# Kernel optimization log

Hardware: AMD Instinct MI355X
Metric: run time of the kernel (lower is better)

The kernel has to match this reference:

```python
import jax, jax.numpy as jnp
import numpy as np

B, S = 4, 4096
D_MODEL = 1024
INDEXER_DIM = 64
LOCAL_WINDOW = 16
MEDIUM_WINDOW = 64
GLOBAL_K = 32
LOCAL_SPARSE = 0.8


def _local_k_schedule(seq_len):
    # Replicates torch: k_local = max(1, int(L * (1 - local_sparse))) with Python float math
    ks = []
    for q in range(seq_len):
        L = min(q + 1, LOCAL_WINDOW)
        ks.append(max(1, int(L * (1.0 - LOCAL_SPARSE))))
    ks = np.asarray(ks, dtype=np.int32)
    return ks, int(ks.max())


def setup_inputs() -> dict:
    key = jax.random.key(0)
    kx, kl, km, kg = jax.random.split(key, 4)
    scale = D_MODEL ** -0.5
    return {
        "x": jax.random.normal(kx, (B, S, D_MODEL), jnp.float32),
        "W_local": jax.random.normal(kl, (INDEXER_DIM, D_MODEL), jnp.float32) * scale,
        "W_medium": jax.random.normal(km, (INDEXER_DIM, D_MODEL), jnp.float32) * scale,
        "W_global": jax.random.normal(kg, (INDEXER_DIM, D_MODEL), jnp.float32) * scale,
    }


def reference(x, W_local, W_medium, W_global):
    Bb, Ss, _ = x.shape
    neg_inf = jnp.array(-jnp.inf, x.dtype)
    zero = jnp.array(0.0, x.dtype)

    lf = x @ W_local.T   # [B,S,i]
    mf = x @ W_medium.T  # computed by the original but DEAD: medium branch never fires
    gf = x @ W_global.T  # [B,S,i]

    mask = jnp.full((Bb, 1, Ss, Ss), -jnp.inf, x.dtype)
    q_ix = jnp.arange(Ss)
    b_ix = jnp.arange(Bb)[:, None, None]
    qq = q_ix[None, :, None]

    # ---- local scale: causal window [max(0, q-W+1), q] ----
    offs = jnp.arange(LOCAL_WINDOW)
    win = q_ix[:, None] - (LOCAL_WINDOW - 1) + offs[None, :]  # [S,W] absolute key positions
    valid = win >= 0
    winc = jnp.clip(win, 0, Ss - 1)
    lwin = lf[:, winc]                                        # [B,S,W,i]
    lscores = jax.nn.relu(jnp.einsum('bqd,bqwd->bqw', lf, lwin))
    lscores = jnp.where(valid[None], lscores, -jnp.inf)
    ks, kmax = _local_k_schedule(Ss)
    _, tl = jax.lax.top_k(lscores, kmax)                      # [B,S,kmax] window-relative
    labs = jnp.take_along_axis(jnp.broadcast_to(winc[None], (Bb, Ss, LOCAL_WINDOW)), tl, axis=-1)
    keep = jnp.arange(kmax)[None, None, :] < jnp.asarray(ks)[None, :, None]  # [1,S,kmax]
    lvals = jnp.where(keep, zero, neg_inf)
    mask = mask.at[b_ix, 0, qq, labs].max(jnp.broadcast_to(lvals, labs.shape))

    # ---- medium scale: DEAD CODE in the original (medium_end == local_end always) ----

    # ---- global scale (active because seq_len > medium_window and global_k > 0) ----
    if Ss > MEDIUM_WINDOW and GLOBAL_K > 0:
        gs = jax.nn.relu(jnp.einsum('bqd,bkd->bqk', gf, gf))  # [B,S,S]
        j = jnp.arange(Ss)[None, :]
        banned = (j <= q_ix[:, None]) & (j >= q_ix[:, None] - (LOCAL_WINDOW - 1))  # [S,S]
        gs = jnp.where(banned[None], -jnp.inf, gs)
        _, tg = jax.lax.top_k(gs, GLOBAL_K)                   # [B,S,Kg]
        mask = mask.at[b_ix, 0, qq, tg].max(jnp.zeros(tg.shape, x.dtype))

    return mask
```

## Files before the change

kernel.cpp:

```cpp
#include <hip/hip_runtime.h>
#include <hip/hip_fp16.h>
#include <cstdint>

#define SEQ 4096
#define NB 4
#define DMODEL 1024
#define ID 64
#define LW 16
#define GK 32
#define TQ 4

#define NEG_INF (-__builtin_inff())
#define MASKED4 0xFBFFFBFFu
#define FMAT (NB * SEQ * ID)

typedef _Float16 f16x8 __attribute__((ext_vector_type(8)));
typedef float f32x4 __attribute__((ext_vector_type(4)));

__global__ __launch_bounds__(256)
void hp_feat_v10(const unsigned short* __restrict__ xu,
                 const unsigned short* __restrict__ Wlu,
                 const unsigned short* __restrict__ Wgu,
                 float* __restrict__ lf, float* __restrict__ gfT)
{
    const int tid = threadIdx.x;
    const int lane = tid & 63, w = tid >> 6;
    const int half = blockIdx.x & 1;
    const long row0 = (long)(blockIdx.x >> 1) * 64;
    const _Float16* xp = (const _Float16*)xu;
    const _Float16* Wp = (const _Float16*)(half ? Wgu : Wlu);

    const int lr = lane & 15;
    const int kg = lane >> 4;

    const _Float16* ap = xp + (row0 + w * 16 + lr) * DMODEL + kg * 8;
    const _Float16* bp = Wp + (long)lr * DMODEL + kg * 8;

    f32x4 acc[4];
#pragma unroll
    for (int ct = 0; ct < 4; ct++) acc[ct] = (f32x4){0.f, 0.f, 0.f, 0.f};

#pragma unroll 4
    for (int k0 = 0; k0 < DMODEL; k0 += 32) {
        f16x8 av = *(const f16x8*)(ap + k0);
#pragma unroll
        for (int ct = 0; ct < 4; ct++) {
            f16x8 bv = *(const f16x8*)(bp + (long)ct * 16 * DMODEL + k0);
            acc[ct] = __builtin_amdgcn_mfma_f32_16x16x32_f16(av, bv, acc[ct], 0, 0, 0);
        }
    }

    if (!half) {
#pragma unroll
        for (int ct = 0; ct < 4; ct++)
#pragma unroll
            for (int r = 0; r < 4; r++)
                lf[(row0 + w * 16 + kg * 4 + r) * ID + ct * 16 + lr] = acc[ct][r];
    } else {
        const int bb = (int)(row0 >> 12), s0 = (int)(row0 & 4095);
#pragma unroll
        for (int ct = 0; ct < 4; ct++) {
            float4 st = make_float4(acc[ct][0], acc[ct][1], acc[ct][2], acc[ct][3]);
            *(float4*)(gfT + ((long)bb * ID + ct * 16 + lr) * SEQ
                           + s0 + w * 16 + kg * 4) = st;
        }
    }
}

__global__ __launch_bounds__(512)
void hp_mask_v10(const float* __restrict__ lf, const float* __restrict__ gfT,
                 unsigned short* __restrict__ out)
{
    __shared__ float qv[TQ][ID];
    __shared__ float lq[TQ][ID];
    __shared__ unsigned long long red[4][8];
    __shared__ unsigned int bitmap[TQ][SEQ / 32];
    __shared__ float lsc[TQ][LW];
    __shared__ unsigned short tm[512];

    const int tid = threadIdx.x;
    const int lane = tid & 63, w = tid >> 6;
    const int bq = blockIdx.x;
    const int b = bq >> 10;
    const int q0 = (bq & 1023) * TQ;
    const float* gTb = gfT + (long)b * ID * SEQ;
    const float* lfb = lf + (long)b * SEQ * ID;

    if (tid < 256) {
        int d = tid >> 2, qi = tid & 3;
        qv[qi][d] = gTb[(long)d * SEQ + q0 + qi];
        int qi2 = tid >> 6, d2 = tid & 63;
        lq[qi2][d2] = lfb[(long)(q0 + qi2) * ID + d2];
    }
    ((unsigned int*)bitmap)[tid] = 0u;
    __syncthreads();

    float acc[2][4][TQ];
#pragma unroll
    for (int c = 0; c < 2; c++)
#pragma unroll
        for (int j = 0; j < 4; j++)
#pragma unroll
            for (int qi = 0; qi < TQ; qi++) acc[c][j][qi] = 0.f;

    const float4* gT4 = (const float4*)gTb;
    for (int d = 0; d < ID; d++) {
        float qd[TQ];
#pragma unroll
        for (int qi = 0; qi < TQ; qi++) qd[qi] = qv[qi][d];
        const float4 ka = gT4[(d << 10) + tid];
        const float4 kb = gT4[(d << 10) + 512 + tid];
#pragma unroll
        for (int qi = 0; qi < TQ; qi++) {
            acc[0][0][qi] = fmaf(ka.x, qd[qi], acc[0][0][qi]);
            acc[0][1][qi] = fmaf(ka.y, qd[qi], acc[0][1][qi]);
            acc[0][2][qi] = fmaf(ka.z, qd[qi], acc[0][2][qi]);
            acc[0][3][qi] = fmaf(ka.w, qd[qi], acc[0][3][qi]);
            acc[1][0][qi] = fmaf(kb.x, qd[qi], acc[1][0][qi]);
            acc[1][1][qi] = fmaf(kb.y, qd[qi], acc[1][1][qi]);
            acc[1][2][qi] = fmaf(kb.z, qd[qi], acc[1][2][qi]);
            acc[1][3][qi] = fmaf(kb.w, qd[qi], acc[1][3][qi]);
        }
    }

#pragma unroll
    for (int c = 0; c < 2; c++)
#pragma unroll
        for (int j = 0; j < 4; j++) {
            const int k = 2048 * c + 4 * tid + j;
#pragma unroll
            for (int qi = 0; qi < TQ; qi++) {
                const int q = q0 + qi;
                const bool banned = (k <= q) && (k >= q - (LW - 1));
                acc[c][j][qi] = banned ? -1.0f : fmaxf(acc[c][j][qi], 0.f);
            }
        }

    unsigned int lo[TQ], hi[TQ];
#pragma unroll
    for (int qi = 0; qi < TQ; qi++) { lo[qi] = 0u; hi[qi] = 0x7F800000u; }

#pragma unroll 1
    for (int it = 0; it < 32; ++it) {
        unsigned long long pc = 0ull;
#pragma unroll
        for (int qi = 0; qi < TQ; qi++) {
            const unsigned int mid = lo[qi] + ((hi[qi] - lo[qi]) >> 1);
            const float tf = __uint_as_float(mid - 1u);
            int cnt = 0;
#pragma unroll
            for (int c = 0; c < 2; c++)
#pragma unroll
                for (int j = 0; j < 4; j++)
                    cnt += __popcll(__ballot(acc[c][j][qi] >= tf));
            pc |= (unsigned long long)(unsigned int)cnt << (16 * qi);
        }
        if (lane == 0) red[it & 1][w] = pc;
        __syncthreads();
        unsigned long long tot = 0ull;
#pragma unroll
        for (int ww = 0; ww < 8; ww++) tot += red[it & 1][ww];
        int conv = 1;
#pragma unroll
        for (int qi = 0; qi < TQ; qi++) {
            const unsigned int mid = lo[qi] + ((hi[qi] - lo[qi]) >> 1);
            const unsigned int cnt =
                (unsigned int)((tot >> (16 * qi)) & 0xFFFFull);
            if (cnt >= GK) lo[qi] = mid; else hi[qi] = mid;
            conv &= (hi[qi] - lo[qi] <= 1u);
        }
        if (conv) break;
    }

    int T[TQ], need[TQ];
    {
        unsigned long long pg = 0ull, pe = 0ull;
#pragma unroll
        for (int qi = 0; qi < TQ; qi++) {
            const float tg = __uint_as_float(lo[qi]);
            const unsigned int eb = lo[qi] - 1u;
            int cg = 0, ce = 0;
#pragma unroll
            for (int c = 0; c < 2; c++)
#pragma unroll
                for (int j = 0; j < 4; j++) {
                    const float v = acc[c][j][qi];
                    cg += __popcll(__ballot(v >= tg));
                    ce += __popcll(__ballot(__float_as_uint(v) == eb));
                }
            pg |= (unsigned long long)(unsigned int)cg << (16 * qi);
            pe |= (unsigned long long)(unsigned int)ce << (16 * qi);
        }
        if (lane == 0) { red[2][w] = pg; red[3][w] = pe; }
        __syncthreads();
        unsigned long long tg = 0ull, te = 0ull;
#pragma unroll
        for (int ww = 0; ww < 8; ww++) { tg += red[2][ww]; te += red[3][ww]; }
#pragma unroll
        for (int qi = 0; qi < TQ; qi++) {
            const int c1 = (int)((tg >> (16 * qi)) & 0xFFFFull);
            T[qi]    = (int)((te >> (16 * qi)) & 0xFFFFull);
            need[qi] = GK - c1;
        }
    }

#pragma unroll
    for (int qi = 0; qi < TQ; qi++) {
        const bool allties = (T[qi] == need[qi]);
        const float tg = __uint_as_float(lo[qi]);
        const unsigned int eb = lo[qi] - 1u;
#pragma unroll
        for (int c = 0; c < 2; c++)
#pragma unroll
            for (int j = 0; j < 4; j++) {
                const float v = acc[c][j][qi];
                const bool sel_ = (v >= tg)
                                | (allties & (__float_as_uint(v) == eb));
                if (sel_) {
                    const int k = 2048 * c + 4 * tid + j;
                    atomicOr(&bitmap[qi][k >> 5], 1u << (k & 31));
                }
            }
    }

#pragma unroll 1
    for (int qi = 0; qi < TQ; qi++) {
        if (T[qi] > need[qi]) {
            const unsigned int eb = lo[qi] - 1u;
            unsigned int m16 = 0u;
#pragma unroll
            for (int c = 0; c < 2; c++)
#pragma unroll
                for (int j = 0; j < 4; j++)
                    if (__float_as_uint(acc[c][j][qi]) == eb)
                        m16 |= 1u << (c * 4 + j);
            tm[tid] = (unsigned short)m16;
            __syncthreads();
            if (tid == 0) {
                int taken = 0;
                for (int c = 0; c < 2 && taken < need[qi]; c++)
                    for (int t = 0; t < 512 && taken < need[qi]; t++) {
                        const unsigned int nib = ((unsigned int)tm[t] >> (c * 4)) & 15u;
                        for (int j = 0; j < 4 && taken < need[qi]; j++)
                            if ((nib >> j) & 1u) {
                                const int k = 2048 * c + 4 * t + j;
                                atomicOr(&bitmap[qi][k >> 5], 1u << (k & 31));
                                taken++;
                            }
                    }
            }
            __syncthreads();
        }
    }

    if (tid < TQ * LW) {
        int qi = tid >> 4, wnd = tid & 15;
        int q = q0 + qi;
        int win = q - (LW - 1) + wnd;
        float v = NEG_INF;
        if (win >= 0) {
            const float4* kr = (const float4*)(lfb + (long)win * ID);
            float s = 0.f;
#pragma unroll
            for (int d = 0; d < 16; d++) {
                float4 kvv = kr[d];
                const float4 qd = *(const float4*)&lq[qi][d * 4];
                s = fmaf(kvv.x, qd.x, s); s = fmaf(kvv.y, qd.y, s);
                s = fmaf(kvv.z, qd.z, s); s = fmaf(kvv.w, qd.w, s);
            }
            v = fmaxf(s, 0.f);
        }
        lsc[qi][wnd] = v;
    }
    __syncthreads();
    if (tid < TQ) {
        int qi = tid, q = q0 + qi;
        int L = (q + 1 < LW) ? q + 1 : LW;
        int ks = L / 5; if (ks < 1) ks = 1;
        for (int t = 0; t < ks; t++) {
            float best = NEG_INF; int bi = 0;
            for (int wnd = 0; wnd < LW; wnd++) {
                float v = lsc[qi][wnd];
                if (v > best) { best = v; bi = wnd; }
            }
            lsc[qi][bi] = NEG_INF;
            const int win = q - (LW - 1) + bi;
            atomicOr(&bitmap[qi][win >> 5], 1u << (win & 31));
        }
    }
    __syncthreads();

    uint4* orow = (uint4*)(out + ((long)b * SEQ + q0) * SEQ);
#pragma unroll
    for (int i = 0; i < TQ * SEQ / 8 / 512; i++) {
        const int li = i * 512 + tid;
        const int qi = li >> 9;
        const int w8 = li & 511;
        const unsigned int bits =
            (bitmap[qi][w8 >> 2] >> ((w8 & 3) * 8)) & 0xFFu;
        uint4 v;
        v.x = MASKED4 & ~(((bits &   1u) ? 0x0000FFFFu : 0u) |
                          ((bits &   2u) ? 0xFFFF0000u : 0u));
        v.y = MASKED4 & ~(((bits &   4u) ? 0x0000FFFFu : 0u) |
                          ((bits &   8u) ? 0xFFFF0000u : 0u));
        v.z = MASKED4 & ~(((bits &  16u) ? 0x0000FFFFu : 0u) |
                          ((bits &  32u) ? 0xFFFF0000u : 0u));
        v.w = MASKED4 & ~(((bits &  64u) ? 0x0000FFFFu : 0u) |
                          ((bits & 128u) ? 0xFFFF0000u : 0u));
        orow[li] = v;
    }
}

extern "C" void kernel_launch(void* const* d_in, const int* in_sizes, int n_in,
                              void* d_out, int out_size, void* d_ws, size_t ws_size,
                              hipStream_t stream) {
    const unsigned short* x  = (const unsigned short*)d_in[0];
    const unsigned short* Wl = (const unsigned short*)d_in[1];
    const unsigned short* Wg = (const unsigned short*)d_in[3];
    unsigned short* out = (unsigned short*)d_out;

    float* lf  = (float*)d_ws;
    float* gfT = lf + (long)FMAT;

    hp_feat_v10<<<(NB * SEQ / 64) * 2, 256, 0, stream>>>(x, Wl, Wg, lf, gfT);
    hp_mask_v10<<<NB * SEQ / TQ, 512, 0, stream>>>(lf, gfT, out);
}
```

Before: 753.5 us.

## Retile feature GEMM per 16 rows, batch score loads, fix bisection trip count

The feature kernel now gives each block 16 rows, and its four waves split the local/global weights and two 32-column chunks. Each x tile is loaded once per block and shared across both projections, and the grid grows to 1024 blocks. The mask kernel unrolls its 64-dim dot product in groups of four, issuing eight float4 key loads and vector query loads from LDS before the FMAs, and requests two blocks per CU through launch bounds. The top-k threshold bisection now always runs 31 iterations with no early-exit convergence check, which removes per-iteration logic but can add iterations for rows that would have converged sooner. The register cap from launch bounds may cause spills.

```diff
diff --git a/kernel.cpp b/kernel.cpp
--- a/kernel.cpp
+++ b/kernel.cpp
@@ -18,57 +18,54 @@
 typedef float f32x4 __attribute__((ext_vector_type(4)));
 
 __global__ __launch_bounds__(256)
-void hp_feat_v10(const unsigned short* __restrict__ xu,
+void hp_feat_v11(const unsigned short* __restrict__ xu,
                  const unsigned short* __restrict__ Wlu,
                  const unsigned short* __restrict__ Wgu,
                  float* __restrict__ lf, float* __restrict__ gfT)
 {
     const int tid = threadIdx.x;
     const int lane = tid & 63, w = tid >> 6;
-    const int half = blockIdx.x & 1;
-    const long row0 = (long)(blockIdx.x >> 1) * 64;
+    const long row0 = (long)blockIdx.x * 16;
+    const int half = w & 1;
+    const int ch = w >> 1;
     const _Float16* xp = (const _Float16*)xu;
     const _Float16* Wp = (const _Float16*)(half ? Wgu : Wlu);
 
     const int lr = lane & 15;
     const int kg = lane >> 4;
 
-    const _Float16* ap = xp + (row0 + w * 16 + lr) * DMODEL + kg * 8;
-    const _Float16* bp = Wp + (long)lr * DMODEL + kg * 8;
-
-    f32x4 acc[4];
-#pragma unroll
-    for (int ct = 0; ct < 4; ct++) acc[ct] = (f32x4){0.f, 0.f, 0.f, 0.f};
+    const _Float16* ap = xp + (row0 + lr) * DMODEL + kg * 8;
+    const _Float16* bp = Wp + (long)(ch * 32 + lr) * DMODEL + kg * 8;
+
+    f32x4 acc0 = (f32x4){0.f, 0.f, 0.f, 0.f};
+    f32x4 acc1 = (f32x4){0.f, 0.f, 0.f, 0.f};
 
 #pragma unroll 4
     for (int k0 = 0; k0 < DMODEL; k0 += 32) {
         f16x8 av = *(const f16x8*)(ap + k0);
-#pragma unroll
-        for (int ct = 0; ct < 4; ct++) {
-            f16x8 bv = *(const f16x8*)(bp + (long)ct * 16 * DMODEL + k0);
-            acc[ct] = __builtin_amdgcn_mfma_f32_16x16x32_f16(av, bv, acc[ct], 0, 0, 0);
-        }
+        f16x8 b0 = *(const f16x8*)(bp + k0);
+        f16x8 b1 = *(const f16x8*)(bp + 16 * DMODEL + k0);
+        acc0 = __builtin_amdgcn_mfma_f32_16x16x32_f16(av, b0, acc0, 0, 0, 0);
+        acc1 = __builtin_amdgcn_mfma_f32_16x16x32_f16(av, b1, acc1, 0, 0, 0);
     }
 
     if (!half) {
 #pragma unroll
-        for (int ct = 0; ct < 4; ct++)
-#pragma unroll
-            for (int r = 0; r < 4; r++)
-                lf[(row0 + w * 16 + kg * 4 + r) * ID + ct * 16 + lr] = acc[ct][r];
+        for (int r = 0; r < 4; r++) {
+            lf[(row0 + kg * 4 + r) * ID + ch * 32 + lr]      = acc0[r];
+            lf[(row0 + kg * 4 + r) * ID + ch * 32 + 16 + lr] = acc1[r];
+        }
     } else {
         const int bb = (int)(row0 >> 12), s0 = (int)(row0 & 4095);
-#pragma unroll
-        for (int ct = 0; ct < 4; ct++) {
-            float4 st = make_float4(acc[ct][0], acc[ct][1], acc[ct][2], acc[ct][3]);
-            *(float4*)(gfT + ((long)bb * ID + ct * 16 + lr) * SEQ
-                           + s0 + w * 16 + kg * 4) = st;
-        }
+        float4 st0 = make_float4(acc0[0], acc0[1], acc0[2], acc0[3]);
+        float4 st1 = make_float4(acc1[0], acc1[1], acc1[2], acc1[3]);
+        *(float4*)(gfT + ((long)bb * ID + ch * 32 + lr) * SEQ + s0 + kg * 4) = st0;
+        *(float4*)(gfT + ((long)bb * ID + ch * 32 + 16 + lr) * SEQ + s0 + kg * 4) = st1;
     }
 }
 
-__global__ __launch_bounds__(512)
-void hp_mask_v10(const float* __restrict__ lf, const float* __restrict__ gfT,
+__global__ __launch_bounds__(512, 2)
+void hp_mask_v11(const float* __restrict__ lf, const float* __restrict__ gfT,
                  unsigned short* __restrict__ out)
 {
     __shared__ float qv[TQ][ID];
@@ -104,22 +101,31 @@
             for (int qi = 0; qi < TQ; qi++) acc[c][j][qi] = 0.f;
 
     const float4* gT4 = (const float4*)gTb;
-    for (int d = 0; d < ID; d++) {
-        float qd[TQ];
-#pragma unroll
-        for (int qi = 0; qi < TQ; qi++) qd[qi] = qv[qi][d];
-        const float4 ka = gT4[(d << 10) + tid];
-        const float4 kb = gT4[(d << 10) + 512 + tid];
-#pragma unroll
-        for (int qi = 0; qi < TQ; qi++) {
-            acc[0][0][qi] = fmaf(ka.x, qd[qi], acc[0][0][qi]);
-            acc[0][1][qi] = fmaf(ka.y, qd[qi], acc[0][1][qi]);
-            acc[0][2][qi] = fmaf(ka.z, qd[qi], acc[0][2][qi]);
-            acc[0][3][qi] = fmaf(ka.w, qd[qi], acc[0][3][qi]);
-            acc[1][0][qi] = fmaf(kb.x, qd[qi], acc[1][0][qi]);
-            acc[1][1][qi] = fmaf(kb.y, qd[qi], acc[1][1][qi]);
-            acc[1][2][qi] = fmaf(kb.z, qd[qi], acc[1][2][qi]);
-            acc[1][3][qi] = fmaf(kb.w, qd[qi], acc[1][3][qi]);
+#pragma unroll 1
+    for (int d0 = 0; d0 < ID; d0 += 4) {
+        float4 ka[4], kb[4], qd4[TQ];
+#pragma unroll
+        for (int dd = 0; dd < 4; dd++) {
+            ka[dd] = gT4[((d0 + dd) << 10) + tid];
+            kb[dd] = gT4[((d0 + dd) << 10) + 512 + tid];
+        }
+#pragma unroll
+        for (int qi = 0; qi < TQ; qi++)
+            qd4[qi] = *(const float4*)&qv[qi][d0];
+#pragma unroll
+        for (int dd = 0; dd < 4; dd++) {
+#pragma unroll
+            for (int qi = 0; qi < TQ; qi++) {
+                const float qd = ((const float*)&qd4[qi])[dd];
+                acc[0][0][qi] = fmaf(ka[dd].x, qd, acc[0][0][qi]);
+                acc[0][1][qi] = fmaf(ka[dd].y, qd, acc[0][1][qi]);
+                acc[0][2][qi] = fmaf(ka[dd].z, qd, acc[0][2][qi]);
+                acc[0][3][qi] = fmaf(ka[dd].w, qd, acc[0][3][qi]);
+                acc[1][0][qi] = fmaf(kb[dd].x, qd, acc[1][0][qi]);
+                acc[1][1][qi] = fmaf(kb[dd].y, qd, acc[1][1][qi]);
+                acc[1][2][qi] = fmaf(kb[dd].z, qd, acc[1][2][qi]);
+                acc[1][3][qi] = fmaf(kb[dd].w, qd, acc[1][3][qi]);
+            }
         }
     }
 
@@ -141,7 +147,7 @@
     for (int qi = 0; qi < TQ; qi++) { lo[qi] = 0u; hi[qi] = 0x7F800000u; }
 
 #pragma unroll 1
-    for (int it = 0; it < 32; ++it) {
+    for (int it = 0; it < 31; ++it) {
         unsigned long long pc = 0ull;
 #pragma unroll
         for (int qi = 0; qi < TQ; qi++) {
@@ -160,16 +166,13 @@
         unsigned long long tot = 0ull;
 #pragma unroll
         for (int ww = 0; ww < 8; ww++) tot += red[it & 1][ww];
-        int conv = 1;
 #pragma unroll
         for (int qi = 0; qi < TQ; qi++) {
             const unsigned int mid = lo[qi] + ((hi[qi] - lo[qi]) >> 1);
             const unsigned int cnt =
                 (unsigned int)((tot >> (16 * qi)) & 0xFFFFull);
             if (cnt >= GK) lo[qi] = mid; else hi[qi] = mid;
-            conv &= (hi[qi] - lo[qi] <= 1u);
-        }
-        if (conv) break;
+        }
     }
 
     int T[TQ], need[TQ];
@@ -322,6 +325,6 @@
     float* lf  = (float*)d_ws;
     float* gfT = lf + (long)FMAT;
 
-    hp_feat_v10<<<(NB * SEQ / 64) * 2, 256, 0, stream>>>(x, Wl, Wg, lf, gfT);
-    hp_mask_v10<<<NB * SEQ / TQ, 512, 0, stream>>>(lf, gfT, out);
+    hp_feat_v11<<<NB * SEQ / 16, 256, 0, stream>>>(x, Wl, Wg, lf, gfT);
+    hp_mask_v11<<<NB * SEQ / TQ, 512, 0, stream>>>(lf, gfT, out);
 }
```

After: 735.3 us. 2.4% less time.

## Fuse feature GEMM and mask kernels into one cooperative persistent kernel

Applied to the files above, without the earlier changes.

Merges the projection GEMM and the mask/top-k kernel into a single cooperative launch of 1024 blocks separated by a grid-wide sync. Each block then processes four query tiles in a persistent loop. It also software-prefetches the next gfT row in the score loop, fixes the binary search at 31 iterations without an early-exit check, and shrinks the tie mask buffer to bytes. This removes one kernel launch and the tail between kernels, but adds grid sync cost and requires all blocks to be co-resident. The GEMM now runs with 16 rows per block and less reuse of the weights.

```diff
diff --git a/kernel.cpp b/kernel.cpp
--- a/kernel.cpp
+++ b/kernel.cpp
@@ -1,6 +1,9 @@
 #include <hip/hip_runtime.h>
 #include <hip/hip_fp16.h>
+#include <hip/hip_cooperative_groups.h>
 #include <cstdint>
+
+namespace cg = cooperative_groups;
 
 #define SEQ 4096
 #define NB 4
@@ -17,297 +20,294 @@
 typedef _Float16 f16x8 __attribute__((ext_vector_type(8)));
 typedef float f32x4 __attribute__((ext_vector_type(4)));
 
-__global__ __launch_bounds__(256)
-void hp_feat_v10(const unsigned short* __restrict__ xu,
-                 const unsigned short* __restrict__ Wlu,
-                 const unsigned short* __restrict__ Wgu,
-                 float* __restrict__ lf, float* __restrict__ gfT)
-{
-    const int tid = threadIdx.x;
-    const int lane = tid & 63, w = tid >> 6;
-    const int half = blockIdx.x & 1;
-    const long row0 = (long)(blockIdx.x >> 1) * 64;
-    const _Float16* xp = (const _Float16*)xu;
-    const _Float16* Wp = (const _Float16*)(half ? Wgu : Wlu);
-
-    const int lr = lane & 15;
-    const int kg = lane >> 4;
-
-    const _Float16* ap = xp + (row0 + w * 16 + lr) * DMODEL + kg * 8;
-    const _Float16* bp = Wp + (long)lr * DMODEL + kg * 8;
-
-    f32x4 acc[4];
-#pragma unroll
-    for (int ct = 0; ct < 4; ct++) acc[ct] = (f32x4){0.f, 0.f, 0.f, 0.f};
-
-#pragma unroll 4
-    for (int k0 = 0; k0 < DMODEL; k0 += 32) {
-        f16x8 av = *(const f16x8*)(ap + k0);
-#pragma unroll
-        for (int ct = 0; ct < 4; ct++) {
-            f16x8 bv = *(const f16x8*)(bp + (long)ct * 16 * DMODEL + k0);
-            acc[ct] = __builtin_amdgcn_mfma_f32_16x16x32_f16(av, bv, acc[ct], 0, 0, 0);
-        }
-    }
-
-    if (!half) {
-#pragma unroll
-        for (int ct = 0; ct < 4; ct++)
-#pragma unroll
-            for (int r = 0; r < 4; r++)
-                lf[(row0 + w * 16 + kg * 4 + r) * ID + ct * 16 + lr] = acc[ct][r];
-    } else {
-        const int bb = (int)(row0 >> 12), s0 = (int)(row0 & 4095);
-#pragma unroll
-        for (int ct = 0; ct < 4; ct++) {
-            float4 st = make_float4(acc[ct][0], acc[ct][1], acc[ct][2], acc[ct][3]);
-            *(float4*)(gfT + ((long)bb * ID + ct * 16 + lr) * SEQ
-                           + s0 + w * 16 + kg * 4) = st;
-        }
-    }
-}
-
-__global__ __launch_bounds__(512)
-void hp_mask_v10(const float* __restrict__ lf, const float* __restrict__ gfT,
-                 unsigned short* __restrict__ out)
+__global__ __launch_bounds__(512, 8)
+void hp_fused_v16(const unsigned short* __restrict__ xu,
+                  const unsigned short* __restrict__ Wlu,
+                  const unsigned short* __restrict__ Wgu,
+                  float* __restrict__ lf, float* __restrict__ gfT,
+                  unsigned short* __restrict__ out)
 {
     __shared__ float qv[TQ][ID];
     __shared__ float lq[TQ][ID];
     __shared__ unsigned long long red[4][8];
     __shared__ unsigned int bitmap[TQ][SEQ / 32];
     __shared__ float lsc[TQ][LW];
-    __shared__ unsigned short tm[512];
+    __shared__ unsigned char tm[512];
 
     const int tid = threadIdx.x;
     const int lane = tid & 63, w = tid >> 6;
-    const int bq = blockIdx.x;
-    const int b = bq >> 10;
-    const int q0 = (bq & 1023) * TQ;
-    const float* gTb = gfT + (long)b * ID * SEQ;
-    const float* lfb = lf + (long)b * SEQ * ID;
-
-    if (tid < 256) {
-        int d = tid >> 2, qi = tid & 3;
-        qv[qi][d] = gTb[(long)d * SEQ + q0 + qi];
-        int qi2 = tid >> 6, d2 = tid & 63;
-        lq[qi2][d2] = lfb[(long)(q0 + qi2) * ID + d2];
+    const int bid = blockIdx.x;
+
+    {
+        const long row0 = (long)bid * 16;
+        const int half = w & 1;
+        const int ch = w >> 1;
+        const _Float16* xp = (const _Float16*)xu;
+        const _Float16* Wp = (const _Float16*)(half ? Wgu : Wlu);
+
+        const int lr = lane & 15;
+        const int kg = lane >> 4;
+
+        const _Float16* ap = xp + (row0 + lr) * DMODEL + kg * 8;
+        const _Float16* bp = Wp + (long)(ch * 16 + lr) * DMODEL + kg * 8;
+
+        f32x4 acc = (f32x4){0.f, 0.f, 0.f, 0.f};
+#pragma unroll 4
+        for (int k0 = 0; k0 < DMODEL; k0 += 32) {
+            f16x8 av = *(const f16x8*)(ap + k0);
+            f16x8 bv = *(const f16x8*)(bp + k0);
+            acc = __builtin_amdgcn_mfma_f32_16x16x32_f16(av, bv, acc, 0, 0, 0);
+        }
+        if (!half) {
+#pragma unroll
+            for (int r = 0; r < 4; r++)
+                lf[(row0 + kg * 4 + r) * ID + ch * 16 + lr] = acc[r];
+        } else {
+            const int bb = (int)(row0 >> 12), s0 = (int)(row0 & 4095);
+            float4 st = make_float4(acc[0], acc[1], acc[2], acc[3]);
+            *(float4*)(gfT + ((long)bb * ID + ch * 16 + lr) * SEQ + s0 + kg * 4) = st;
+        }
     }
-    ((unsigned int*)bitmap)[tid] = 0u;
-    __syncthreads();
-
-    float acc[2][4][TQ];
-#pragma unroll
-    for (int c = 0; c < 2; c++)
-#pragma unroll
-        for (int j = 0; j < 4; j++)
-#pragma unroll
-            for (int qi = 0; qi < TQ; qi++) acc[c][j][qi] = 0.f;
-
-    const float4* gT4 = (const float4*)gTb;
-    for (int d = 0; d < ID; d++) {
-        float qd[TQ];
-#pragma unroll
-        for (int qi = 0; qi < TQ; qi++) qd[qi] = qv[qi][d];
-        const float4 ka = gT4[(d << 10) + tid];
-        const float4 kb = gT4[(d << 10) + 512 + tid];
+
+    __threadfence();
+    cg::this_grid().sync();
+
+#pragma unroll 1
+    for (int r = 0; r < 4; ++r) {
+        const int g = r * 1024 + bid;
+        const int b = g >> 10;
+        const int q0 = (g & 1023) * TQ;
+        const float* gTb = gfT + (long)b * ID * SEQ;
+        const float* lfb = lf + (long)b * SEQ * ID;
+
+        if (tid < 256) {
+            int d = tid >> 2, qi = tid & 3;
+            qv[qi][d] = gTb[(long)d * SEQ + q0 + qi];
+            int qi2 = tid >> 6, d2 = tid & 63;
+            lq[qi2][d2] = lfb[(long)(q0 + qi2) * ID + d2];
+        }
+        ((unsigned int*)bitmap)[tid] = 0u;
+        __syncthreads();
+
+        float acc[2][4][TQ];
+#pragma unroll
+        for (int c = 0; c < 2; c++)
+#pragma unroll
+            for (int j = 0; j < 4; j++)
+#pragma unroll
+                for (int qi = 0; qi < TQ; qi++) acc[c][j][qi] = 0.f;
+
+        const float4* gT4 = (const float4*)gTb;
+        float4 ka = gT4[tid], kb = gT4[512 + tid];
+#pragma unroll 1
+        for (int d = 0; d < ID; d++) {
+            float4 na, nb;
+            if (d + 1 < ID) {
+                na = gT4[((d + 1) << 10) + tid];
+                nb = gT4[((d + 1) << 10) + 512 + tid];
+            }
+            float qd[TQ];
+#pragma unroll
+            for (int qi = 0; qi < TQ; qi++) qd[qi] = qv[qi][d];
+#pragma unroll
+            for (int qi = 0; qi < TQ; qi++) {
+                acc[0][0][qi] = fmaf(ka.x, qd[qi], acc[0][0][qi]);
+                acc[0][1][qi] = fmaf(ka.y, qd[qi], acc[0][1][qi]);
+                acc[0][2][qi] = fmaf(ka.z, qd[qi], acc[0][2][qi]);
+                acc[0][3][qi] = fmaf(ka.w, qd[qi], acc[0][3][qi]);
+                acc[1][0][qi] = fmaf(kb.x, qd[qi], acc[1][0][qi]);
+                acc[1][1][qi] = fmaf(kb.y, qd[qi], acc[1][1][qi]);
+                acc[1][2][qi] = fmaf(kb.z, qd[qi], acc[1][2][qi]);
+                acc[1][3][qi] = fmaf(kb.w, qd[qi], acc[1][3][qi]);
+            }
+            ka = na; kb = nb;
+        }
+
+#pragma unroll
+        for (int c = 0; c < 2; c++)
+#pragma unroll
+            for (int j = 0; j < 4; j++) {
+                const int k = 2048 * c + 4 * tid + j;
+#pragma unroll
+                for (int qi = 0; qi < TQ; qi++) {
+                    const int q = q0 + qi;
+                    const bool banned = (k <= q) && (k >= q - (LW - 1));
+                    acc[c][j][qi] = banned ? -1.0f : fmaxf(acc[c][j][qi], 0.f);
+                }
+            }
+
+        unsigned int lo[TQ], hi[TQ];
+#pragma unroll
+        for (int qi = 0; qi < TQ; qi++) { lo[qi] = 0u; hi[qi] = 0x7F800000u; }
+
+#pragma unroll 1
+        for (int it = 0; it < 31; ++it) {
+            unsigned long long pc = 0ull;
+#pragma unroll
+            for (int qi = 0; qi < TQ; qi++) {
+                const unsigned int mid = lo[qi] + ((hi[qi] - lo[qi]) >> 1);
+                const float tf = __uint_as_float(mid - 1u);
+                int cnt = 0;
+#pragma unroll
+                for (int c = 0; c < 2; c++)
+#pragma unroll
+                    for (int j = 0; j < 4; j++)
+                        cnt += __popcll(__ballot(acc[c][j][qi] >= tf));
+                pc |= (unsigned long long)(unsigned int)cnt << (16 * qi);
+            }
+            if (lane == 0) red[it & 1][w] = pc;
+            __syncthreads();
+            unsigned long long tot = 0ull;
+#pragma unroll
+            for (int ww = 0; ww < 8; ww++) tot += red[it & 1][ww];
+#pragma unroll
+            for (int qi = 0; qi < TQ; qi++) {
+                const unsigned int mid = lo[qi] + ((hi[qi] - lo[qi]) >> 1);
+                const unsigned int cnt =
+                    (unsigned int)((tot >> (16 * qi)) & 0xFFFFull);
+                if (cnt >= GK) lo[qi] = mid; else hi[qi] = mid;
+            }
+        }
+
+        int T[TQ], need[TQ];
+        {
+            unsigned long long pg = 0ull, pe = 0ull;
+#pragma unroll
+            for (int qi = 0; qi < TQ; qi++) {
+                const float tg = __uint_as_float(lo[qi]);
+                const unsigned int eb = lo[qi] - 1u;
+                int cg = 0, ce = 0;
+#pragma unroll
+                for (int c = 0; c < 2; c++)
+#pragma unroll
+                    for (int j = 0; j < 4; j++) {
+                        const float v = acc[c][j][qi];
+                        cg += __popcll(__ballot(v >= tg));
+                        ce += __popcll(__ballot(__float_as_uint(v) == eb));
+                    }
+                pg |= (unsigned long long)(unsigned int)cg << (16 * qi);
+                pe |= (unsigned long long)(unsigned int)ce << (16 * qi);
+            }
+            if (lane == 0) { red[2][w] = pg; red[3][w] = pe; }
+            __syncthreads();
+            unsigned long long tg = 0ull, te = 0ull;
+#pragma unroll
+            for (int ww = 0; ww < 8; ww++) { tg += red[2][ww]; te += red[3][ww]; }
+#pragma unroll
+            for (int qi = 0; qi < TQ; qi++) {
+                const int c1 = (int)((tg >> (16 * qi)) & 0xFFFFull);
+                T[qi]    = (int)((te >> (16 * qi)) & 0xFFFFull);
+                need[qi] = GK - c1;
+            }
+        }
+
 #pragma unroll
         for (int qi = 0; qi < TQ; qi++) {
-            acc[0][0][qi] = fmaf(ka.x, qd[qi], acc[0][0][qi]);
-            acc[0][1][qi] = fmaf(ka.y, qd[qi], acc[0][1][qi]);
-            acc[0][2][qi] = fmaf(ka.z, qd[qi], acc[0][2][qi]);
-            acc[0][3][qi] = fmaf(ka.w, qd[qi], acc[0][3][qi]);
-            acc[1][0][qi] = fmaf(kb.x, qd[qi], acc[1][0][qi]);
-            acc[1][1][qi] = fmaf(kb.y, qd[qi], acc[1][1][qi]);
-            acc[1][2][qi] = fmaf(kb.z, qd[qi], acc[1][2][qi]);
-            acc[1][3][qi] = fmaf(kb.w, qd[qi], acc[1][3][qi]);
-        }
-    }
-
-#pragma unroll
-    for (int c = 0; c < 2; c++)
-#pragma unroll
-        for (int j = 0; j < 4; j++) {
-            const int k = 2048 * c + 4 * tid + j;
-#pragma unroll
-            for (int qi = 0; qi < TQ; qi++) {
-                const int q = q0 + qi;
-                const bool banned = (k <= q) && (k >= q - (LW - 1));
-                acc[c][j][qi] = banned ? -1.0f : fmaxf(acc[c][j][qi], 0.f);
-            }
-        }
-
-    unsigned int lo[TQ], hi[TQ];
-#pragma unroll
-    for (int qi = 0; qi < TQ; qi++) { lo[qi] = 0u; hi[qi] = 0x7F800000u; }
-
-#pragma unroll 1
-    for (int it = 0; it < 32; ++it) {
-        unsigned long long pc = 0ull;
-#pragma unroll
-        for (int qi = 0; qi < TQ; qi++) {
-            const unsigned int mid = lo[qi] + ((hi[qi] - lo[qi]) >> 1);
-            const float tf = __uint_as_float(mid - 1u);
-            int cnt = 0;
-#pragma unroll
-            for (int c = 0; c < 2; c++)
-#pragma unroll
-                for (int j = 0; j < 4; j++)
-                    cnt += __popcll(__ballot(acc[c][j][qi] >= tf));
-            pc |= (unsigned long long)(unsigned int)cnt << (16 * qi);
-        }
-        if (lane == 0) red[it & 1][w] = pc;
-        __syncthreads();
-        unsigned long long tot = 0ull;
-#pragma unroll
-        for (int ww = 0; ww < 8; ww++) tot += red[it & 1][ww];
-        int conv = 1;
-#pragma unroll
-        for (int qi = 0; qi < TQ; qi++) {
-            const unsigned int mid = lo[qi] + ((hi[qi] - lo[qi]) >> 1);
-            const unsigned int cnt =
-                (unsigned int)((tot >> (16 * qi)) & 0xFFFFull);
-            if (cnt >= GK) lo[qi] = mid; else hi[qi] = mid;
-            conv &= (hi[qi] - lo[qi] <= 1u);
-        }
-        if (conv) break;
-    }
-
-    int T[TQ], need[TQ];
-    {
-        unsigned long long pg = 0ull, pe = 0ull;
-#pragma unroll
-        for (int qi = 0; qi < TQ; qi++) {
+            const bool allties = (T[qi] == need[qi]);
             const float tg = __uint_as_float(lo[qi]);
             const unsigned int eb = lo[qi] - 1u;
-            int cg = 0, ce = 0;
 #pragma unroll
             for (int c = 0; c < 2; c++)
 #pragma unroll
                 for (int j = 0; j < 4; j++) {
                     const float v = acc[c][j][qi];
-                    cg += __popcll(__ballot(v >= tg));
-                    ce += __popcll(__ballot(__float_as_uint(v) == eb));
-                }
-            pg |= (unsigned long long)(unsigned int)cg << (16 * qi);
-            pe |= (unsigned long long)(unsigned int)ce << (16 * qi);
-        }
-        if (lane == 0) { red[2][w] = pg; red[3][w] = pe; }
+                    const bool sel_ = (v >= tg)
+                                    | (allties & (__float_as_uint(v) == eb));
+                    if (sel_) {
+                        const int k = 2048 * c + 4 * tid + j;
+                        atomicOr(&bitmap[qi][k >> 5], 1u << (k & 31));
+                    }
+                }
+        }
+
+#pragma unroll 1
+        for (int qi = 0; qi < TQ; qi++) {
+            if (T[qi] > need[qi]) {
+                const unsigned int eb = lo[qi] - 1u;
+                unsigned int m8 = 0u;
+#pragma unroll
+                for (int c = 0; c < 2; c++)
+#pragma unroll
+                    for (int j = 0; j < 4; j++)
+                        if (__float_as_uint(acc[c][j][qi]) == eb)
+                            m8 |= 1u << (c * 4 + j);
+                tm[tid] = (unsigned char)m8;
+                __syncthreads();
+                if (tid == 0) {
+                    int taken = 0;
+                    for (int c = 0; c < 2 && taken < need[qi]; c++)
+                        for (int t = 0; t < 512 && taken < need[qi]; t++) {
+                            const unsigned int nib =
+                                ((unsigned int)tm[t] >> (c * 4)) & 15u;
+                            for (int j = 0; j < 4 && taken < need[qi]; j++)
+                                if ((nib >> j) & 1u) {
+                                    const int k = 2048 * c + 4 * t + j;
+                                    atomicOr(&bitmap[qi][k >> 5], 1u << (k & 31));
+                                    taken++;
+                                }
+                        }
+                }
+                __syncthreads();
+            }
+        }
+
+        if (tid < TQ * LW) {
+            int qi = tid >> 4, wnd = tid & 15;
+            int q = q0 + qi;
+            int win = q - (LW - 1) + wnd;
+            float v = NEG_INF;
+            if (win >= 0) {
+                const float4* kr = (const float4*)(lfb + (long)win * ID);
+                float s = 0.f;
+#pragma unroll
+                for (int d = 0; d < 16; d++) {
+                    float4 kvv = kr[d];
+                    const float4 qd = *(const float4*)&lq[qi][d * 4];
+                    s = fmaf(kvv.x, qd.x, s); s = fmaf(kvv.y, qd.y, s);
+                    s = fmaf(kvv.z, qd.z, s); s = fmaf(kvv.w, qd.w, s);
+                }
+                v = fmaxf(s, 0.f);
+            }
+            lsc[qi][wnd] = v;
+        }
         __syncthreads();
-        unsigned long long tg = 0ull, te = 0ull;
-#pragma unroll
-        for (int ww = 0; ww < 8; ww++) { tg += red[2][ww]; te += red[3][ww]; }
-#pragma unroll
-        for (int qi = 0; qi < TQ; qi++) {
-            const int c1 = (int)((tg >> (16 * qi)) & 0xFFFFull);
-            T[qi]    = (int)((te >> (16 * qi)) & 0xFFFFull);
-            need[qi] = GK - c1;
-        }
-    }
-
-#pragma unroll
-    for (int qi = 0; qi < TQ; qi++) {
-        const bool allties = (T[qi] == need[qi]);
-        const float tg = __uint_as_float(lo[qi]);
-        const unsigned int eb = lo[qi] - 1u;
-#pragma unroll
-        for (int c = 0; c < 2; c++)
-#pragma unroll
-            for (int j = 0; j < 4; j++) {
-                const float v = acc[c][j][qi];
-                const bool sel_ = (v >= tg)
-                                | (allties & (__float_as_uint(v) == eb));
-                if (sel_) {
-                    const int k = 2048 * c + 4 * tid + j;
-                    atomicOr(&bitmap[qi][k >> 5], 1u << (k & 31));
-                }
-            }
-    }
-
-#pragma unroll 1
-    for (int qi = 0; qi < TQ; qi++) {
-        if (T[qi] > need[qi]) {
-            const unsigned int eb = lo[qi] - 1u;
-            unsigned int m16 = 0u;
-#pragma unroll
-            for (int c = 0; c < 2; c++)
-#pragma unroll
-                for (int j = 0; j < 4; j++)
-                    if (__float_as_uint(acc[c][j][qi]) == eb)
-                        m16 |= 1u << (c * 4 + j);
-            tm[tid] = (unsigned short)m16;
-            __syncthreads();
-            if (tid == 0) {
-                int taken = 0;
-                for (int c = 0; c < 2 && taken < need[qi]; c++)
-                    for (int t = 0; t < 512 && taken < need[qi]; t++) {
-                        const unsigned int nib = ((unsigned int)tm[t] >> (c * 4)) & 15u;
-                        for (int j = 0; j < 4 && taken < need[qi]; j++)
-                            if ((nib >> j) & 1u) {
-                                const int k = 2048 * c + 4 * t + j;
-                                atomicOr(&bitmap[qi][k >> 5], 1u << (k & 31));
-                                taken++;
-                            }
-                    }
-            }
-            __syncthreads();
-        }
-    }
-
-    if (tid < TQ * LW) {
-        int qi = tid >> 4, wnd = tid & 15;
-        int q = q0 + qi;
-        int win = q - (LW - 1) + wnd;
-        float v = NEG_INF;
-        if (win >= 0) {
-            const float4* kr = (const float4*)(lfb + (long)win * ID);
-            float s = 0.f;
-#pragma unroll
-            for (int d = 0; d < 16; d++) {
-                float4 kvv = kr[d];
-                const float4 qd = *(const float4*)&lq[qi][d * 4];
-                s = fmaf(kvv.x, qd.x, s); s = fmaf(kvv.y, qd.y, s);
-                s = fmaf(kvv.z, qd.z, s); s = fmaf(kvv.w, qd.w, s);
-            }
-            v = fmaxf(s, 0.f);
-        }
-        lsc[qi][wnd] = v;
-    }
-    __syncthreads();
-    if (tid < TQ) {
-        int qi = tid, q = q0 + qi;
-        int L = (q + 1 < LW) ? q + 1 : LW;
-        int ks = L / 5; if (ks < 1) ks = 1;
-        for (int t = 0; t < ks; t++) {
-            float best = NEG_INF; int bi = 0;
-            for (int wnd = 0; wnd < LW; wnd++) {
-                float v = lsc[qi][wnd];
-                if (v > best) { best = v; bi = wnd; }
-            }
-            lsc[qi][bi] = NEG_INF;
-            const int win = q - (LW - 1) + bi;
-            atomicOr(&bitmap[qi][win >> 5], 1u << (win & 31));
-        }
-    }
-    __syncthreads();
-
-    uint4* orow = (uint4*)(out + ((long)b * SEQ + q0) * SEQ);
-#pragma unroll
-    for (int i = 0; i < TQ * SEQ / 8 / 512; i++) {
-        const int li = i * 512 + tid;
-        const int qi = li >> 9;
-        const int w8 = li & 511;
-        const unsigned int bits =
-            (bitmap[qi][w8 >> 2] >> ((w8 & 3) * 8)) & 0xFFu;
-        uint4 v;
-        v.x = MASKED4 & ~(((bits &   1u) ? 0x0000FFFFu : 0u) |
-                          ((bits &   2u) ? 0xFFFF0000u : 0u));
-        v.y = MASKED4 & ~(((bits &   4u) ? 0x0000FFFFu : 0u) |
-                          ((bits &   8u) ? 0xFFFF0000u : 0u));
-        v.z = MASKED4 & ~(((bits &  16u) ? 0x0000FFFFu : 0u) |
-                          ((bits &  32u) ? 0xFFFF0000u : 0u));
-        v.w = MASKED4 & ~(((bits &  64u) ? 0x0000FFFFu : 0u) |
-                          ((bits & 128u) ? 0xFFFF0000u : 0u));
-        orow[li] = v;
+        if (tid < TQ) {
+            int qi = tid, q = q0 + qi;
+            int L = (q + 1 < LW) ? q + 1 : LW;
+            int ks = L / 5; if (ks < 1) ks = 1;
+            for (int t = 0; t < ks; t++) {
+                float best = NEG_INF; int bi = 0;
+                for (int wnd = 0; wnd < LW; wnd++) {
+                    float v = lsc[qi][wnd];
+                    if (v > best) { best = v; bi = wnd; }
+                }
+                lsc[qi][bi] = NEG_INF;
+                const int win = q - (LW - 1) + bi;
+                atomicOr(&bitmap[qi][win >> 5], 1u << (win & 31));
+            }
+        }
+        __syncthreads();
+
+        uint4* orow = (uint4*)(out + ((long)b * SEQ + q0) * SEQ);
+#pragma unroll
+        for (int i = 0; i < TQ * SEQ / 8 / 512; i++) {
+            const int li = i * 512 + tid;
+            const int qi = li >> 9;
+            const int w8 = li & 511;
+            const unsigned int bits =
+                (bitmap[qi][w8 >> 2] >> ((w8 & 3) * 8)) & 0xFFu;
+            uint4 v;
+            v.x = MASKED4 & ~(((bits &   1u) ? 0x0000FFFFu : 0u) |
+                              ((bits &   2u) ? 0xFFFF0000u : 0u));
+            v.y = MASKED4 & ~(((bits &   4u) ? 0x0000FFFFu : 0u) |
+                              ((bits &   8u) ? 0xFFFF0000u : 0u));
+            v.z = MASKED4 & ~(((bits &  16u) ? 0x0000FFFFu : 0u) |
+                              ((bits &  32u) ? 0xFFFF0000u : 0u));
+            v.w = MASKED4 & ~(((bits &  64u) ? 0x0000FFFFu : 0u) |
+                              ((bits & 128u) ? 0xFFFF0000u : 0u));
+            orow[li] = v;
+        }
+        __syncthreads();
     }
 }
 
@@ -322,6 +322,9 @@
     float* lf  = (float*)d_ws;
     float* gfT = lf + (long)FMAT;
 
-    hp_feat_v10<<<(NB * SEQ / 64) * 2, 256, 0, stream>>>(x, Wl, Wg, lf, gfT);
-    hp_mask_v10<<<NB * SEQ / TQ, 512, 0, stream>>>(lf, gfT, out);
+    void* kargs[] = {(void*)&x, (void*)&Wl, (void*)&Wg,
+                     (void*)&lf, (void*)&gfT, (void*)&out};
+    hipLaunchCooperativeKernel((const void*)hp_fused_v16,
+                               dim3(NB * SEQ / 16), dim3(512),
+                               kargs, 0, stream);
 }
```

New measurement: 2.177 ms. 189% more time.
